# Kernel optimization log

Measured on AMD Instinct MI355X. Metric: run time of the kernel, lower is better.

Reference implementation:

```python
import jax, jax.numpy as jnp
import numpy as np
from jax import lax

H = 128

def _lstm_gates(x, h, c, w_ih, w_hh, b_ih, b_hh):
    # PyTorch gate order: i, f, g, o
    g = x @ w_ih.T + h @ w_hh.T + b_ih + b_hh
    i, f, gg, o = jnp.split(g, 4, axis=-1)
    c_new = jax.nn.sigmoid(f) * c + jax.nn.sigmoid(i) * jnp.tanh(gg)
    h_new = jax.nn.sigmoid(o) * jnp.tanh(c_new)
    return h_new, c_new

def _lstm_layer(x_btF, w_ih, w_hh, b_ih, b_hh):
    B = x_btF.shape[0]
    h0 = jnp.zeros((B, H), x_btF.dtype)
    c0 = jnp.zeros((B, H), x_btF.dtype)
    def step(carry, xt):
        h, c = carry
        h, c = _lstm_gates(xt, h, c, w_ih, w_hh, b_ih, b_hh)
        return (h, c), h
    (h_T, c_T), ys = lax.scan(step, (h0, c0), jnp.swapaxes(x_btF, 0, 1))
    return jnp.swapaxes(ys, 0, 1), h_T, c_T

def setup_inputs() -> dict:
    key = jax.random.key(0)
    ks = jax.random.split(key, 20)
    B, T, D, P = 4096, 200, 2, 3
    s = 1.0 / np.sqrt(H)
    u = lambda k, shp: jax.random.uniform(k, shp, jnp.float32, -s, s)
    return {
        'x_hist': jax.random.normal(ks[0], (B, T, D), jnp.float32),
        'params': jax.random.normal(ks[1], (B, P), jnp.float32),
        'pred_len': 200,
        'w_ih0': u(ks[2], (4 * H, D)), 'w_hh0': u(ks[3], (4 * H, H)),
        'b_ih0': u(ks[4], (4 * H,)), 'b_hh0': u(ks[5], (4 * H,)),
        'w_ih1': u(ks[6], (4 * H, H)), 'w_hh1': u(ks[7], (4 * H, H)),
        'b_ih1': u(ks[8], (4 * H,)), 'b_hh1': u(ks[9], (4 * H,)),
        'dec_w_ih': u(ks[10], (4 * H, D + P)), 'dec_w_hh': u(ks[11], (4 * H, H)),
        'dec_b_ih': u(ks[12], (4 * H,)), 'dec_b_hh': u(ks[13], (4 * H,)),
        'proj_w': u(ks[14], (H, P)), 'proj_b': u(ks[15], (H,)),
        'out_w': u(ks[16], (2, H)), 'out_b': u(ks[17], (2,)),
    }

def reference(x_hist, params, pred_len, w_ih0, w_hh0, b_ih0, b_hh0,
              w_ih1, w_hh1, b_ih1, b_hh1, dec_w_ih, dec_w_hh, dec_b_ih,
              dec_b_hh, proj_w, proj_b, out_w, out_b):
    # 2-layer encoder LSTM; only last layer's final (h, c) are used
    y1, _, _ = _lstm_layer(x_hist, w_ih0, w_hh0, b_ih0, b_hh0)
    _, h_n, c_n = _lstm_layer(y1, w_ih1, w_hh1, b_ih1, b_hh1)
    h = h_n + params @ proj_w.T + proj_b
    c = c_n
    cur = x_hist[:, -1, :]
    def step(carry, _):
        h, c, cur = carry
        inp = jnp.concatenate([cur, params], axis=-1)
        h, c = _lstm_gates(inp, h, c, dec_w_ih, dec_w_hh, dec_b_ih, dec_b_hh)
        cur = h @ out_w.T + out_b
        return (h, c, cur), cur
    _, preds = lax.scan(step, (h, c, cur), None, length=pred_len)
    return jnp.swapaxes(preds, 0, 1)  # [B, pred_len, 2]
```

## Files before the change

### kernel.cpp

```cpp
#include <hip/hip_runtime.h>
#include <stdint.h>

typedef __bf16 bf16x8 __attribute__((ext_vector_type(8)));
typedef float  f32x4  __attribute__((ext_vector_type(4)));

#define PRED   200
#define TSTEPS 200
#define NBLK   256
#define ABUFB  8192
#define L1_A_OFF   131072
#define L1_ST_OFF  (131072 + 2*ABUFB)
#define LDS_L1     (131072 + 3*ABUFB)
#define LDS_SMALL  (2*ABUFB)

#define STATE_FLOATS ((size_t)NBLK*4*2048)

__device__ __forceinline__ float sigm(float x){ return 1.0f/(1.0f+__expf(-x)); }
__device__ __forceinline__ float tanhx(float x){
  float t=__expf(-2.0f*fabsf(x)); float y=(1.0f-t)/(1.0f+t); return copysignf(y,x);
}
__device__ __forceinline__ bf16x8 hi8(float4 a, float4 b){
  bf16x8 r; r[0]=(__bf16)a.x; r[1]=(__bf16)a.y; r[2]=(__bf16)a.z; r[3]=(__bf16)a.w;
  r[4]=(__bf16)b.x; r[5]=(__bf16)b.y; r[6]=(__bf16)b.z; r[7]=(__bf16)b.w; return r;
}
__device__ __forceinline__ bf16x8 lo8(float4 a, float4 b, bf16x8 h){
  bf16x8 r;
  r[0]=(__bf16)(a.x-(float)h[0]); r[1]=(__bf16)(a.y-(float)h[1]);
  r[2]=(__bf16)(a.z-(float)h[2]); r[3]=(__bf16)(a.w-(float)h[3]);
  r[4]=(__bf16)(b.x-(float)h[4]); r[5]=(__bf16)(b.y-(float)h[5]);
  r[6]=(__bf16)(b.z-(float)h[6]); r[7]=(__bf16)(b.w-(float)h[7]); return r;
}
__device__ __forceinline__ uint16_t bfbits(__bf16 x){ union{__bf16 b; uint16_t u;} v; v.b=x; return v.u; }
__device__ __forceinline__ __bf16 bits2bf(uint16_t u){ union{uint16_t u; __bf16 b;} v; v.u=u; return v.b; }
#define MFMA(A,B,C) __builtin_amdgcn_mfma_f32_16x16x32_bf16((A),(B),(C),0,0,0)

__device__ __forceinline__ int aoff(int row, int col){
  return row*512 + ((((col>>3) ^ (row&7)) << 4) | ((col&7)<<1));
}
__device__ __forceinline__ int frdoff(int c, int qd, int kt, int plane){
  return c*512 + (((((kt<<2)+qd) ^ (c&7)) | (plane<<4)) << 4);
}

__global__ void __launch_bounds__(512,1)
k_l0(const float* __restrict__ xh, const float* __restrict__ wih0,
     const float* __restrict__ whh0, const float* __restrict__ bih0,
     const float* __restrict__ bhh0, float* __restrict__ wsf,
     int chunkStart, int chunkLen, unsigned long long stageFloats)
{
  extern __shared__ char smem[];
  const int tid=threadIdx.x, wv=tid>>6, l=tid&63, c=l&15, qd=l>>4;
  const int hc=wv*16+c, blk=blockIdx.x, r0=blk*16;
  float* stf = wsf + stageFloats;
  bf16x8 whi[16], wlo[16];
  #pragma unroll
  for (int tt=0;tt<4;++tt)
    #pragma unroll
    for (int kt=0;kt<4;++kt){
      const float* s=whh0+(size_t)(tt*128+hc)*128+kt*32+qd*8;
      float4 a=*(const float4*)s, b=*(const float4*)(s+4);
      whi[tt*4+kt]=hi8(a,b); wlo[tt*4+kt]=lo8(a,b,whi[tt*4+kt]);
    }
  float b0[4], w0x[4], w0y[4];
  #pragma unroll
  for (int tt=0;tt<4;++tt){
    int g=tt*128+hc;
    b0[tt]=bih0[g]+bhh0[g]; w0x[tt]=wih0[2*g]; w0y[tt]=wih0[2*g+1];
  }
  float c0[4];
  {
    char* B1=smem+ABUFB;
    const float* hst=stf+(size_t)(blk*4+0)*2048;
    const float* cst=stf+(size_t)(blk*4+1)*2048;
    #pragma unroll
    for (int i=0;i<4;++i){
      int e=tid*4+i, row=e>>7, col=e&127;
      float v=0.f; if(chunkStart) v=hst[e];
      __bf16 h=(__bf16)v;
      *(__bf16*)(B1+aoff(row,col))=h;
      *(__bf16*)(B1+aoff(row,col+128))=(__bf16)(v-(float)h);
    }
    #pragma unroll
    for (int j=0;j<4;++j){ float v=0.f; if(chunkStart) v=cst[(qd*4+j)*128+hc]; c0[j]=v; }
  }
  __syncthreads();
  for (int t=0;t<chunkLen;++t){
    const int p=t&1, tg=chunkStart+t;
    float2 xv[4];
    #pragma unroll
    for (int j=0;j<4;++j) xv[j]=*(const float2*)(xh+(size_t)(r0+qd*4+j)*400+tg*2);
    f32x4 acc[4];
    #pragma unroll
    for (int tt=0;tt<4;++tt) acc[tt]=(f32x4){b0[tt],b0[tt],b0[tt],b0[tt]};
    const char* Ar=smem+(size_t)(1-p)*ABUFB;
    #pragma unroll
    for (int kt=0;kt<4;++kt){
      bf16x8 ah=*(const bf16x8*)(Ar+frdoff(c,qd,kt,0));
      bf16x8 al=*(const bf16x8*)(Ar+frdoff(c,qd,kt,1));
      #pragma unroll
      for (int tt=0;tt<4;++tt){
        acc[tt]=MFMA(ah,whi[tt*4+kt],acc[tt]);
        acc[tt]=MFMA(al,whi[tt*4+kt],acc[tt]);
        acc[tt]=MFMA(ah,wlo[tt*4+kt],acc[tt]);
      }
    }
    char* Aw=smem+(size_t)p*ABUFB;
    uint32_t* h0o=(uint32_t*)(wsf+((size_t)t*NBLK+blk)*2048);
    #pragma unroll
    for (int j=0;j<4;++j){
      float gi=acc[0][j]+xv[j].x*w0x[0]+xv[j].y*w0y[0];
      float gf=acc[1][j]+xv[j].x*w0x[1]+xv[j].y*w0y[1];
      float gg=acc[2][j]+xv[j].x*w0x[2]+xv[j].y*w0y[2];
      float go=acc[3][j]+xv[j].x*w0x[3]+xv[j].y*w0y[3];
      float cn=sigm(gf)*c0[j]+sigm(gi)*tanhx(gg); c0[j]=cn;
      float hn=sigm(go)*tanhx(cn);
      int row=qd*4+j;
      __bf16 hh=(__bf16)hn;
      __bf16 hl=(__bf16)(hn-(float)hh);
      *(__bf16*)(Aw+aoff(row,hc))=hh;
      *(__bf16*)(Aw+aoff(row,hc+128))=hl;
      h0o[row*128+hc]=(uint32_t)bfbits(hh) | ((uint32_t)bfbits(hl)<<16);
      if (t==chunkLen-1){
        stf[(size_t)(blk*4+0)*2048+row*128+hc]=hn;
        stf[(size_t)(blk*4+1)*2048+row*128+hc]=cn;
      }
    }
    __syncthreads();
  }
}

__global__ void __launch_bounds__(512,1)
k_l1(const float* __restrict__ wih1, const float* __restrict__ whh1,
     const float* __restrict__ bih1, const float* __restrict__ bhh1,
     float* __restrict__ wsf, int chunkStart, int chunkLen,
     unsigned long long stageFloats)
{
  extern __shared__ char smem[];
  const int tid=threadIdx.x, wv=tid>>6, l=tid&63, c=l&15, qd=l>>4;
  const int hc=wv*16+c, blk=blockIdx.x;
  float* stf = wsf + stageFloats;
  #pragma unroll
  for (int i=0;i<16;++i){
    int f=i*8+wv, ntg=f>>2, kt=f&3;
    int g=(ntg&3)*128+(ntg>>2)*16+c, k=kt*32+qd*8;
    const float* s=wih1+g*128+k;
    *(bf16x8*)(smem+f*1024+l*16)=hi8(*(const float4*)s,*(const float4*)(s+4));
  }
  bf16x8 wil[16], whh[16], whl[16];
  #pragma unroll
  for (int tt=0;tt<4;++tt)
    #pragma unroll
    for (int kt=0;kt<4;++kt){
      const float* s=wih1+(size_t)(tt*128+hc)*128+kt*32+qd*8;
      float4 a=*(const float4*)s, b=*(const float4*)(s+4);
      wil[tt*4+kt]=lo8(a,b,hi8(a,b));
      const float* s2=whh1+(size_t)(tt*128+hc)*128+kt*32+qd*8;
      float4 a2=*(const float4*)s2, b2=*(const float4*)(s2+4);
      bf16x8 h2=hi8(a2,b2);
      whh[tt*4+kt]=h2; whl[tt*4+kt]=lo8(a2,b2,h2);
    }
  float b1v[4];
  #pragma unroll
  for (int tt=0;tt<4;++tt){ int g=tt*128+hc; b1v[tt]=bih1[g]+bhh1[g]; }
  float c1[4];
  {
    char* B1=smem+L1_A_OFF+ABUFB;
    const float* hst=stf+(size_t)(blk*4+2)*2048;
    const float* cst=stf+(size_t)(blk*4+3)*2048;
    #pragma unroll
    for (int i=0;i<4;++i){
      int e=tid*4+i, row=e>>7, col=e&127;
      float v=0.f; if(chunkStart) v=hst[e];
      __bf16 h=(__bf16)v;
      *(__bf16*)(B1+aoff(row,col))=h;
      *(__bf16*)(B1+aoff(row,col+128))=(__bf16)(v-(float)h);
    }
    #pragma unroll
    for (int j=0;j<4;++j){ float v=0.f; if(chunkStart) v=cst[(qd*4+j)*128+hc]; c1[j]=v; }
  }
  uint4 r4=*(const uint4*)((const uint32_t*)(wsf+((size_t)0*NBLK+blk)*2048)+tid*4);
  __syncthreads();
  for (int t=0;t<chunkLen;++t){
    const int p=t&1;
    {
      char* ST=smem+L1_ST_OFF;
      int e=tid*4, row=e>>7, col=e&127;
      uint32_t uu[4]={r4.x,r4.y,r4.z,r4.w};
      #pragma unroll
      for (int i=0;i<4;++i){
        *(__bf16*)(ST+aoff(row,col+i))=bits2bf((uint16_t)(uu[i]&0xFFFFu));
        *(__bf16*)(ST+aoff(row,col+i+128))=bits2bf((uint16_t)(uu[i]>>16));
      }
    }
    if (t+1<chunkLen) r4=*(const uint4*)((const uint32_t*)(wsf+((size_t)(t+1)*NBLK+blk)*2048)+tid*4);
    __syncthreads();
    f32x4 acc[4];
    #pragma unroll
    for (int tt=0;tt<4;++tt) acc[tt]=(f32x4){b1v[tt],b1v[tt],b1v[tt],b1v[tt]};
    const char* Ar=smem+L1_A_OFF+(size_t)(1-p)*ABUFB;
    const char* Sr=smem+L1_ST_OFF;
    #pragma unroll
    for (int kt=0;kt<4;++kt){
      bf16x8 a0h=*(const bf16x8*)(Sr+frdoff(c,qd,kt,0));
      bf16x8 a0l=*(const bf16x8*)(Sr+frdoff(c,qd,kt,1));
      bf16x8 a1h=*(const bf16x8*)(Ar+frdoff(c,qd,kt,0));
      bf16x8 a1l=*(const bf16x8*)(Ar+frdoff(c,qd,kt,1));
      #pragma unroll
      for (int tt=0;tt<4;++tt){
        bf16x8 bh=*(const bf16x8*)(smem+(size_t)((wv*4+tt)*4+kt)*1024+l*16);
        acc[tt]=MFMA(a0h,bh,acc[tt]);
        acc[tt]=MFMA(a0l,bh,acc[tt]);
        acc[tt]=MFMA(a0h,wil[tt*4+kt],acc[tt]);
        acc[tt]=MFMA(a1h,whh[tt*4+kt],acc[tt]);
        acc[tt]=MFMA(a1l,whh[tt*4+kt],acc[tt]);
        acc[tt]=MFMA(a1h,whl[tt*4+kt],acc[tt]);
      }
    }
    char* Aw=smem+L1_A_OFF+(size_t)p*ABUFB;
    #pragma unroll
    for (int j=0;j<4;++j){
      float cn=sigm(acc[1][j])*c1[j]+sigm(acc[0][j])*tanhx(acc[2][j]); c1[j]=cn;
      float hn=sigm(acc[3][j])*tanhx(cn);
      int row=qd*4+j;
      __bf16 hh=(__bf16)hn;
      *(__bf16*)(Aw+aoff(row,hc))=hh;
      *(__bf16*)(Aw+aoff(row,hc+128))=(__bf16)(hn-(float)hh);
      if (t==chunkLen-1){
        stf[(size_t)(blk*4+2)*2048+row*128+hc]=hn;
        stf[(size_t)(blk*4+3)*2048+row*128+hc]=cn;
      }
    }
    __syncthreads();
  }
}

__global__ void __launch_bounds__(512,1)
k_dec(const float* __restrict__ xh, const float* __restrict__ pprm,
      const float* __restrict__ dwihp, const float* __restrict__ dwhh,
      const float* __restrict__ dbih, const float* __restrict__ dbhh,
      const float* __restrict__ pw, const float* __restrict__ pb,
      const float* __restrict__ ow, const float* __restrict__ ob,
      const float* __restrict__ wsf, float* __restrict__ out,
      unsigned long long stageFloats)
{
  extern __shared__ char smem[];
  const int tid=threadIdx.x, wv=tid>>6, l=tid&63, c=l&15, qd=l>>4;
  const int hc=wv*16+c, blk=blockIdx.x, r0=blk*16;
  const float* stf = wsf + stageFloats;
  bf16x8 whi[16], wlo[16];
  #pragma unroll
  for (int tt=0;tt<4;++tt)
    #pragma unroll
    for (int kt=0;kt<4;++kt){
      const float* s=dwhh+(size_t)(tt*128+hc)*128+kt*32+qd*8;
      float4 a=*(const float4*)s, b=*(const float4*)(s+4);
      whi[tt*4+kt]=hi8(a,b); wlo[tt*4+kt]=lo8(a,b,whi[tt*4+kt]);
    }
  bf16x8 owh[4], owl[4];
  #pragma unroll
  for (int kt=0;kt<4;++kt){
    int cc=(c<2)?c:0;
    const float* s=ow+cc*128+kt*32+qd*8;
    float4 a=*(const float4*)s, b=*(const float4*)(s+4);
    if (c>=2){ a=(float4){0,0,0,0}; b=(float4){0,0,0,0}; }
    owh[kt]=hi8(a,b); owl[kt]=lo8(a,b,owh[kt]);
  }
  float ob0=ob[0], ob1=ob[1];
  float prm[4][3];
  #pragma unroll
  for (int j=0;j<4;++j){
    size_t r=(size_t)(r0+qd*4+j);
    prm[j][0]=pprm[r*3+0]; prm[j][1]=pprm[r*3+1]; prm[j][2]=pprm[r*3+2];
  }
  float pt[4][4], dw0[4], dw1[4];
  #pragma unroll
  for (int tt=0;tt<4;++tt){
    int g=tt*128+hc;
    float db=dbih[g]+dbhh[g];
    dw0[tt]=dwihp[g*5+0]; dw1[tt]=dwihp[g*5+1];
    #pragma unroll
    for (int j=0;j<4;++j)
      pt[tt][j]=db+prm[j][0]*dwihp[g*5+2]+prm[j][1]*dwihp[g*5+3]+prm[j][2]*dwihp[g*5+4];
  }
  const float* h1s=stf+(size_t)(blk*4+2)*2048;
  const float* c1s=stf+(size_t)(blk*4+3)*2048;
  float c1[4], cx0[4], cx1[4];
  {
    float prj0=pw[hc*3+0], prj1=pw[hc*3+1], prj2=pw[hc*3+2], prjb=pb[hc];
    char* B0=smem;
    #pragma unroll
    for (int j=0;j<4;++j){
      int row=qd*4+j;
      float hd=h1s[row*128+hc]+prm[j][0]*prj0+prm[j][1]*prj1+prm[j][2]*prj2+prjb;
      __bf16 h=(__bf16)hd;
      *(__bf16*)(B0+aoff(row,hc))=h;
      *(__bf16*)(B0+aoff(row,hc+128))=(__bf16)(hd-(float)h);
      c1[j]=c1s[row*128+hc];
      float2 xx=*(const float2*)(xh+(size_t)(r0+row)*400+398);
      cx0[j]=xx.x; cx1[j]=xx.y;
    }
  }
  __syncthreads();
  for (int s=0;s<PRED;++s){
    const int q=s&1;
    const char* Ar=smem+(size_t)q*ABUFB;
    f32x4 acc[4], accPV={0.f,0.f,0.f,0.f};
    #pragma unroll
    for (int tt=0;tt<4;++tt) acc[tt]=(f32x4){pt[tt][0],pt[tt][1],pt[tt][2],pt[tt][3]};
    #pragma unroll
    for (int kt=0;kt<4;++kt){
      bf16x8 ah=*(const bf16x8*)(Ar+frdoff(c,qd,kt,0));
      bf16x8 al=*(const bf16x8*)(Ar+frdoff(c,qd,kt,1));
      #pragma unroll
      for (int tt=0;tt<4;++tt){
        acc[tt]=MFMA(ah,whi[tt*4+kt],acc[tt]);
        acc[tt]=MFMA(al,whi[tt*4+kt],acc[tt]);
        acc[tt]=MFMA(ah,wlo[tt*4+kt],acc[tt]);
      }
      accPV=MFMA(ah,owh[kt],accPV);
      accPV=MFMA(al,owh[kt],accPV);
      accPV=MFMA(ah,owl[kt],accPV);
    }
    float cur0[4], cur1[4];
    #pragma unroll
    for (int j=0;j<4;++j){
      float pv0=__shfl(accPV[j], (l&48),   64);
      float pv1=__shfl(accPV[j], (l&48)|1, 64);
      cur0[j]= s ? (pv0+ob0) : cx0[j];
      cur1[j]= s ? (pv1+ob1) : cx1[j];
    }
    if (s && wv==0 && c<2){
      float obv=c?ob1:ob0;
      #pragma unroll
      for (int j=0;j<4;++j)
        out[(size_t)(r0+qd*4+j)*400+(s-1)*2+c]=accPV[j]+obv;
    }
    char* Aw=smem+(size_t)(1-q)*ABUFB;
    #pragma unroll
    for (int j=0;j<4;++j){
      float gi=acc[0][j]+cur0[j]*dw0[0]+cur1[j]*dw1[0];
      float gf=acc[1][j]+cur0[j]*dw0[1]+cur1[j]*dw1[1];
      float gg=acc[2][j]+cur0[j]*dw0[2]+cur1[j]*dw1[2];
      float go=acc[3][j]+cur0[j]*dw0[3]+cur1[j]*dw1[3];
      float cn=sigm(gf)*c1[j]+sigm(gi)*tanhx(gg); c1[j]=cn;
      float hn=sigm(go)*tanhx(cn);
      int row=qd*4+j;
      __bf16 hh=(__bf16)hn;
      *(__bf16*)(Aw+aoff(row,hc))=hh;
      *(__bf16*)(Aw+aoff(row,hc+128))=(__bf16)(hn-(float)hh);
    }
    __syncthreads();
  }
  {
    const char* Ar=smem+(size_t)(PRED&1)*ABUFB;
    f32x4 accPV={0.f,0.f,0.f,0.f};
    #pragma unroll
    for (int kt=0;kt<4;++kt){
      bf16x8 ah=*(const bf16x8*)(Ar+frdoff(c,qd,kt,0));
      bf16x8 al=*(const bf16x8*)(Ar+frdoff(c,qd,kt,1));
      accPV=MFMA(ah,owh[kt],accPV);
      accPV=MFMA(al,owh[kt],accPV);
      accPV=MFMA(ah,owl[kt],accPV);
    }
    if (wv==0 && c<2){
      float obv=c?ob1:ob0;
      #pragma unroll
      for (int j=0;j<4;++j)
        out[(size_t)(r0+qd*4+j)*400+(PRED-1)*2+c]=accPV[j]+obv;
    }
  }
}

extern "C" void kernel_launch(void* const* d_in, const int* in_sizes, int n_in,
                              void* d_out, int out_size, void* d_ws, size_t ws_size,
                              hipStream_t stream)
{
  (void)out_size;
  const int base = (n_in >= 19 && in_sizes[2] == 1) ? 3 : 2;
  const float* xh   = (const float*)d_in[0];
  const float* prm  = (const float*)d_in[1];
  const float* wih0 = (const float*)d_in[base+0];
  const float* whh0 = (const float*)d_in[base+1];
  const float* bih0 = (const float*)d_in[base+2];
  const float* bhh0 = (const float*)d_in[base+3];
  const float* wih1 = (const float*)d_in[base+4];
  const float* whh1 = (const float*)d_in[base+5];
  const float* bih1 = (const float*)d_in[base+6];
  const float* bhh1 = (const float*)d_in[base+7];
  const float* dwih = (const float*)d_in[base+8];
  const float* dwhh = (const float*)d_in[base+9];
  const float* dbih = (const float*)d_in[base+10];
  const float* dbhh = (const float*)d_in[base+11];
  const float* pw   = (const float*)d_in[base+12];
  const float* pb   = (const float*)d_in[base+13];
  const float* ow   = (const float*)d_in[base+14];
  const float* ob   = (const float*)d_in[base+15];
  float* wsf = (float*)d_ws;

  size_t wsFloats = ws_size / 4;
  size_t avail = (wsFloats > STATE_FLOATS) ? (wsFloats - STATE_FLOATS) : 0;
  int chunkLen = (int)(avail / ((size_t)NBLK * 2048));
  if (chunkLen > 50) chunkLen = 50;
  if (chunkLen < 1)  chunkLen = 1;
  unsigned long long stageFloats = (unsigned long long)chunkLen * NBLK * 2048;

  hipFuncSetAttribute((const void*)k_l1, hipFuncAttributeMaxDynamicSharedMemorySize, LDS_L1);

  for (int k0 = 0; k0 < TSTEPS; k0 += chunkLen){
    int len = chunkLen; if (k0 + len > TSTEPS) len = TSTEPS - k0;
    k_l0<<<NBLK,512,LDS_SMALL,stream>>>(xh, wih0, whh0, bih0, bhh0, wsf, k0, len, stageFloats);
    k_l1<<<NBLK,512,LDS_L1,stream>>>(wih1, whh1, bih1, bhh1, wsf, k0, len, stageFloats);
  }
  k_dec<<<NBLK,512,LDS_SMALL,stream>>>(xh, prm, dwih, dwhh, dbih, dbhh,
                                       pw, pb, ow, ob, wsf, (float*)d_out, stageFloats);
}
```

Baseline: 2.032 ms.

## Fold decoder output projection into recurrent weights and split MFMA accumulator chains

The decoder now folds the output projection (out_w, out_b) into the recurrent weight matrix and bias, so each step no longer waits on a per-step projection MFMA and shuffle. Projections of the stored bf16 hidden states are computed later in batched sweeps, and a one-time correction term handles the first step's real input. Layer 1 reads layer-0 outputs straight from global memory into registers instead of staging them through LDS with an extra barrier. Both encoder layers and the decoder split their accumulators into two independent chains to shorten MFMA dependency latency. Chunk length is raised to cover all timesteps, which cuts kernel launches when workspace allows. The folded weights and the bf16-only stored hidden state for projection change numerics somewhat.

```diff
diff --git a/kernel.cpp b/kernel.cpp
--- a/kernel.cpp
+++ b/kernel.cpp
@@ -9,8 +9,7 @@
 #define NBLK   256
 #define ABUFB  8192
 #define L1_A_OFF   131072
-#define L1_ST_OFF  (131072 + 2*ABUFB)
-#define LDS_L1     (131072 + 3*ABUFB)
+#define LDS_L1     (131072 + 2*ABUFB)
 #define LDS_SMALL  (2*ABUFB)
 
 #define STATE_FLOATS ((size_t)NBLK*4*2048)
@@ -88,9 +87,9 @@
     float2 xv[4];
     #pragma unroll
     for (int j=0;j<4;++j) xv[j]=*(const float2*)(xh+(size_t)(r0+qd*4+j)*400+tg*2);
-    f32x4 acc[4];
-    #pragma unroll
-    for (int tt=0;tt<4;++tt) acc[tt]=(f32x4){b0[tt],b0[tt],b0[tt],b0[tt]};
+    f32x4 accA[4], accB[4];
+    #pragma unroll
+    for (int tt=0;tt<4;++tt){ accA[tt]=(f32x4){b0[tt],b0[tt],b0[tt],b0[tt]}; accB[tt]=(f32x4){0.f,0.f,0.f,0.f}; }
     const char* Ar=smem+(size_t)(1-p)*ABUFB;
     #pragma unroll
     for (int kt=0;kt<4;++kt){
@@ -98,19 +97,20 @@
       bf16x8 al=*(const bf16x8*)(Ar+frdoff(c,qd,kt,1));
       #pragma unroll
       for (int tt=0;tt<4;++tt){
-        acc[tt]=MFMA(ah,whi[tt*4+kt],acc[tt]);
-        acc[tt]=MFMA(al,whi[tt*4+kt],acc[tt]);
-        acc[tt]=MFMA(ah,wlo[tt*4+kt],acc[tt]);
+        f32x4* tgt=(kt<2)?&accA[tt]:&accB[tt];
+        *tgt=MFMA(ah,whi[tt*4+kt],*tgt);
+        *tgt=MFMA(al,whi[tt*4+kt],*tgt);
+        *tgt=MFMA(ah,wlo[tt*4+kt],*tgt);
       }
     }
     char* Aw=smem+(size_t)p*ABUFB;
     uint32_t* h0o=(uint32_t*)(wsf+((size_t)t*NBLK+blk)*2048);
     #pragma unroll
     for (int j=0;j<4;++j){
-      float gi=acc[0][j]+xv[j].x*w0x[0]+xv[j].y*w0y[0];
-      float gf=acc[1][j]+xv[j].x*w0x[1]+xv[j].y*w0y[1];
-      float gg=acc[2][j]+xv[j].x*w0x[2]+xv[j].y*w0y[2];
-      float go=acc[3][j]+xv[j].x*w0x[3]+xv[j].y*w0y[3];
+      float gi=accA[0][j]+accB[0][j]+xv[j].x*w0x[0]+xv[j].y*w0y[0];
+      float gf=accA[1][j]+accB[1][j]+xv[j].x*w0x[1]+xv[j].y*w0y[1];
+      float gg=accA[2][j]+accB[2][j]+xv[j].x*w0x[2]+xv[j].y*w0y[2];
+      float go=accA[3][j]+accB[3][j]+xv[j].x*w0x[3]+xv[j].y*w0y[3];
       float cn=sigm(gf)*c0[j]+sigm(gi)*tanhx(gg); c0[j]=cn;
       float hn=sigm(go)*tanhx(cn);
       int row=qd*4+j;
@@ -177,49 +177,58 @@
     #pragma unroll
     for (int j=0;j<4;++j){ float v=0.f; if(chunkStart) v=cst[(qd*4+j)*128+hc]; c1[j]=v; }
   }
-  uint4 r4=*(const uint4*)((const uint32_t*)(wsf+((size_t)0*NBLK+blk)*2048)+tid*4);
   __syncthreads();
   for (int t=0;t<chunkLen;++t){
     const int p=t&1;
-    {
-      char* ST=smem+L1_ST_OFF;
-      int e=tid*4, row=e>>7, col=e&127;
-      uint32_t uu[4]={r4.x,r4.y,r4.z,r4.w};
-      #pragma unroll
-      for (int i=0;i<4;++i){
-        *(__bf16*)(ST+aoff(row,col+i))=bits2bf((uint16_t)(uu[i]&0xFFFFu));
-        *(__bf16*)(ST+aoff(row,col+i+128))=bits2bf((uint16_t)(uu[i]>>16));
-      }
-    }
-    if (t+1<chunkLen) r4=*(const uint4*)((const uint32_t*)(wsf+((size_t)(t+1)*NBLK+blk)*2048)+tid*4);
-    __syncthreads();
-    f32x4 acc[4];
-    #pragma unroll
-    for (int tt=0;tt<4;++tt) acc[tt]=(f32x4){b1v[tt],b1v[tt],b1v[tt],b1v[tt]};
+    const uint32_t* h0p=(const uint32_t*)(wsf)+((size_t)t*NBLK+blk)*2048 + c*128 + qd*8;
+    uint4 L[8];
+    #pragma unroll
+    for (int kt=0;kt<4;++kt){
+      L[kt*2]  =*(const uint4*)(h0p+kt*32);
+      L[kt*2+1]=*(const uint4*)(h0p+kt*32+4);
+    }
+    f32x4 acc1[4], acc0[4];
+    #pragma unroll
+    for (int tt=0;tt<4;++tt){ acc1[tt]=(f32x4){b1v[tt],b1v[tt],b1v[tt],b1v[tt]}; acc0[tt]=(f32x4){0.f,0.f,0.f,0.f}; }
     const char* Ar=smem+L1_A_OFF+(size_t)(1-p)*ABUFB;
-    const char* Sr=smem+L1_ST_OFF;
-    #pragma unroll
-    for (int kt=0;kt<4;++kt){
-      bf16x8 a0h=*(const bf16x8*)(Sr+frdoff(c,qd,kt,0));
-      bf16x8 a0l=*(const bf16x8*)(Sr+frdoff(c,qd,kt,1));
+    #pragma unroll
+    for (int kt=0;kt<4;++kt){
       bf16x8 a1h=*(const bf16x8*)(Ar+frdoff(c,qd,kt,0));
       bf16x8 a1l=*(const bf16x8*)(Ar+frdoff(c,qd,kt,1));
       #pragma unroll
       for (int tt=0;tt<4;++tt){
+        acc1[tt]=MFMA(a1h,whh[tt*4+kt],acc1[tt]);
+        acc1[tt]=MFMA(a1l,whh[tt*4+kt],acc1[tt]);
+        acc1[tt]=MFMA(a1h,whl[tt*4+kt],acc1[tt]);
+      }
+    }
+    #pragma unroll
+    for (int kt=0;kt<4;++kt){
+      uint32_t u[8]={L[kt*2].x,L[kt*2].y,L[kt*2].z,L[kt*2].w,
+                     L[kt*2+1].x,L[kt*2+1].y,L[kt*2+1].z,L[kt*2+1].w};
+      bf16x8 a0h, a0l;
+      #pragma unroll
+      for (int i=0;i<8;++i){
+        a0h[i]=bits2bf((uint16_t)(u[i]&0xFFFFu));
+        a0l[i]=bits2bf((uint16_t)(u[i]>>16));
+      }
+      #pragma unroll
+      for (int tt=0;tt<4;++tt){
         bf16x8 bh=*(const bf16x8*)(smem+(size_t)((wv*4+tt)*4+kt)*1024+l*16);
-        acc[tt]=MFMA(a0h,bh,acc[tt]);
-        acc[tt]=MFMA(a0l,bh,acc[tt]);
-        acc[tt]=MFMA(a0h,wil[tt*4+kt],acc[tt]);
-        acc[tt]=MFMA(a1h,whh[tt*4+kt],acc[tt]);
-        acc[tt]=MFMA(a1l,whh[tt*4+kt],acc[tt]);
-        acc[tt]=MFMA(a1h,whl[tt*4+kt],acc[tt]);
+        acc0[tt]=MFMA(a0h,bh,acc0[tt]);
+        acc0[tt]=MFMA(a0l,bh,acc0[tt]);
+        acc0[tt]=MFMA(a0h,wil[tt*4+kt],acc0[tt]);
       }
     }
     char* Aw=smem+L1_A_OFF+(size_t)p*ABUFB;
     #pragma unroll
     for (int j=0;j<4;++j){
-      float cn=sigm(acc[1][j])*c1[j]+sigm(acc[0][j])*tanhx(acc[2][j]); c1[j]=cn;
-      float hn=sigm(acc[3][j])*tanhx(cn);
+      float gi=acc0[0][j]+acc1[0][j];
+      float gf=acc0[1][j]+acc1[1][j];
+      float gg=acc0[2][j]+acc1[2][j];
+      float go=acc0[3][j]+acc1[3][j];
+      float cn=sigm(gf)*c1[j]+sigm(gi)*tanhx(gg); c1[j]=cn;
+      float hn=sigm(go)*tanhx(cn);
       int row=qd*4+j;
       __bf16 hh=(__bf16)hn;
       *(__bf16*)(Aw+aoff(row,hc))=hh;
@@ -239,20 +248,44 @@
       const float* __restrict__ dbih, const float* __restrict__ dbhh,
       const float* __restrict__ pw, const float* __restrict__ pb,
       const float* __restrict__ ow, const float* __restrict__ ob,
-      const float* __restrict__ wsf, float* __restrict__ out,
-      unsigned long long stageFloats)
+      float* __restrict__ wsf, float* __restrict__ out,
+      unsigned long long stageFloats, int hcap)
 {
   extern __shared__ char smem[];
   const int tid=threadIdx.x, wv=tid>>6, l=tid&63, c=l&15, qd=l>>4;
   const int hc=wv*16+c, blk=blockIdx.x, r0=blk*16;
   const float* stf = wsf + stageFloats;
+  float ob0=ob[0], ob1=ob[1];
+  float prm[4][3];
+  #pragma unroll
+  for (int j=0;j<4;++j){
+    size_t r=(size_t)(r0+qd*4+j);
+    prm[j][0]=pprm[r*3+0]; prm[j][1]=pprm[r*3+1]; prm[j][2]=pprm[r*3+2];
+  }
+  float ptF[4][4], dw0[4], dw1[4];
+  #pragma unroll
+  for (int tt=0;tt<4;++tt){
+    int g=tt*128+hc;
+    float db=dbih[g]+dbhh[g];
+    dw0[tt]=dwihp[g*5+0]; dw1[tt]=dwihp[g*5+1];
+    #pragma unroll
+    for (int j=0;j<4;++j)
+      ptF[tt][j]=db+prm[j][0]*dwihp[g*5+2]+prm[j][1]*dwihp[g*5+3]+prm[j][2]*dwihp[g*5+4]
+                 +dw0[tt]*ob0+dw1[tt]*ob1;
+  }
   bf16x8 whi[16], wlo[16];
   #pragma unroll
   for (int tt=0;tt<4;++tt)
     #pragma unroll
     for (int kt=0;kt<4;++kt){
-      const float* s=dwhh+(size_t)(tt*128+hc)*128+kt*32+qd*8;
-      float4 a=*(const float4*)s, b=*(const float4*)(s+4);
+      int g=tt*128+hc, k=kt*32+qd*8;
+      float4 a=*(const float4*)(dwhh+(size_t)g*128+k), b=*(const float4*)(dwhh+(size_t)g*128+k+4);
+      float4 o0a=*(const float4*)(ow+k),     o0b=*(const float4*)(ow+k+4);
+      float4 o1a=*(const float4*)(ow+128+k), o1b=*(const float4*)(ow+128+k+4);
+      a.x+=dw0[tt]*o0a.x+dw1[tt]*o1a.x; a.y+=dw0[tt]*o0a.y+dw1[tt]*o1a.y;
+      a.z+=dw0[tt]*o0a.z+dw1[tt]*o1a.z; a.w+=dw0[tt]*o0a.w+dw1[tt]*o1a.w;
+      b.x+=dw0[tt]*o0b.x+dw1[tt]*o1b.x; b.y+=dw0[tt]*o0b.y+dw1[tt]*o1b.y;
+      b.z+=dw0[tt]*o0b.z+dw1[tt]*o1b.z; b.w+=dw0[tt]*o0b.w+dw1[tt]*o1b.w;
       whi[tt*4+kt]=hi8(a,b); wlo[tt*4+kt]=lo8(a,b,whi[tt*4+kt]);
     }
   bf16x8 owh[4], owl[4];
@@ -263,23 +296,6 @@
     float4 a=*(const float4*)s, b=*(const float4*)(s+4);
     if (c>=2){ a=(float4){0,0,0,0}; b=(float4){0,0,0,0}; }
     owh[kt]=hi8(a,b); owl[kt]=lo8(a,b,owh[kt]);
-  }
-  float ob0=ob[0], ob1=ob[1];
-  float prm[4][3];
-  #pragma unroll
-  for (int j=0;j<4;++j){
-    size_t r=(size_t)(r0+qd*4+j);
-    prm[j][0]=pprm[r*3+0]; prm[j][1]=pprm[r*3+1]; prm[j][2]=pprm[r*3+2];
-  }
-  float pt[4][4], dw0[4], dw1[4];
-  #pragma unroll
-  for (int tt=0;tt<4;++tt){
-    int g=tt*128+hc;
-    float db=dbih[g]+dbhh[g];
-    dw0[tt]=dwihp[g*5+0]; dw1[tt]=dwihp[g*5+1];
-    #pragma unroll
-    for (int j=0;j<4;++j)
-      pt[tt][j]=db+prm[j][0]*dwihp[g*5+2]+prm[j][1]*dwihp[g*5+3]+prm[j][2]*dwihp[g*5+4];
   }
   const float* h1s=stf+(size_t)(blk*4+2)*2048;
   const float* c1s=stf+(size_t)(blk*4+3)*2048;
@@ -300,72 +316,85 @@
     }
   }
   __syncthreads();
+  float corr0[4], corr1[4];
+  {
+    const char* Ar=smem;
+    f32x4 pv={0.f,0.f,0.f,0.f};
+    #pragma unroll
+    for (int kt=0;kt<4;++kt){
+      bf16x8 ah=*(const bf16x8*)(Ar+frdoff(c,qd,kt,0));
+      bf16x8 al=*(const bf16x8*)(Ar+frdoff(c,qd,kt,1));
+      pv=MFMA(ah,owh[kt],pv); pv=MFMA(al,owh[kt],pv); pv=MFMA(ah,owl[kt],pv);
+    }
+    #pragma unroll
+    for (int j=0;j<4;++j){
+      float p0=__shfl(pv[j], (l&48),   64);
+      float p1=__shfl(pv[j], (l&48)|1, 64);
+      corr0[j]=cx0[j]-(p0+ob0);
+      corr1[j]=cx1[j]-(p1+ob1);
+    }
+  }
+  uint16_t* hstp=(uint16_t*)wsf;
+  int sweepBase=0;
   for (int s=0;s<PRED;++s){
     const int q=s&1;
     const char* Ar=smem+(size_t)q*ABUFB;
-    f32x4 acc[4], accPV={0.f,0.f,0.f,0.f};
-    #pragma unroll
-    for (int tt=0;tt<4;++tt) acc[tt]=(f32x4){pt[tt][0],pt[tt][1],pt[tt][2],pt[tt][3]};
+    f32x4 aA[4], aB[4];
+    #pragma unroll
+    for (int tt=0;tt<4;++tt){ aA[tt]=(f32x4){ptF[tt][0],ptF[tt][1],ptF[tt][2],ptF[tt][3]}; aB[tt]=(f32x4){0.f,0.f,0.f,0.f}; }
     #pragma unroll
     for (int kt=0;kt<4;++kt){
       bf16x8 ah=*(const bf16x8*)(Ar+frdoff(c,qd,kt,0));
       bf16x8 al=*(const bf16x8*)(Ar+frdoff(c,qd,kt,1));
       #pragma unroll
       for (int tt=0;tt<4;++tt){
-        acc[tt]=MFMA(ah,whi[tt*4+kt],acc[tt]);
-        acc[tt]=MFMA(al,whi[tt*4+kt],acc[tt]);
-        acc[tt]=MFMA(ah,wlo[tt*4+kt],acc[tt]);
-      }
-      accPV=MFMA(ah,owh[kt],accPV);
-      accPV=MFMA(al,owh[kt],accPV);
-      accPV=MFMA(ah,owl[kt],accPV);
-    }
-    float cur0[4], cur1[4];
+        f32x4* tgt=(kt<2)?&aA[tt]:&aB[tt];
+        *tgt=MFMA(ah,whi[tt*4+kt],*tgt);
+        *tgt=MFMA(al,whi[tt*4+kt],*tgt);
+        *tgt=MFMA(ah,wlo[tt*4+kt],*tgt);
+      }
+    }
+    char* Aw=smem+(size_t)(1-q)*ABUFB;
+    uint16_t* hs=hstp+(size_t)(s-sweepBase)*((size_t)NBLK*2048)+(size_t)blk*2048;
     #pragma unroll
     for (int j=0;j<4;++j){
-      float pv0=__shfl(accPV[j], (l&48),   64);
-      float pv1=__shfl(accPV[j], (l&48)|1, 64);
-      cur0[j]= s ? (pv0+ob0) : cx0[j];
-      cur1[j]= s ? (pv1+ob1) : cx1[j];
-    }
-    if (s && wv==0 && c<2){
-      float obv=c?ob1:ob0;
-      #pragma unroll
-      for (int j=0;j<4;++j)
-        out[(size_t)(r0+qd*4+j)*400+(s-1)*2+c]=accPV[j]+obv;
-    }
-    char* Aw=smem+(size_t)(1-q)*ABUFB;
-    #pragma unroll
-    for (int j=0;j<4;++j){
-      float gi=acc[0][j]+cur0[j]*dw0[0]+cur1[j]*dw1[0];
-      float gf=acc[1][j]+cur0[j]*dw0[1]+cur1[j]*dw1[1];
-      float gg=acc[2][j]+cur0[j]*dw0[2]+cur1[j]*dw1[2];
-      float go=acc[3][j]+cur0[j]*dw0[3]+cur1[j]*dw1[3];
+      float gi=aA[0][j]+aB[0][j];
+      float gf=aA[1][j]+aB[1][j];
+      float gg=aA[2][j]+aB[2][j];
+      float go=aA[3][j]+aB[3][j];
+      if (s==0){
+        gi+=corr0[j]*dw0[0]+corr1[j]*dw1[0];
+        gf+=corr0[j]*dw0[1]+corr1[j]*dw1[1];
+        gg+=corr0[j]*dw0[2]+corr1[j]*dw1[2];
+        go+=corr0[j]*dw0[3]+corr1[j]*dw1[3];
+      }
       float cn=sigm(gf)*c1[j]+sigm(gi)*tanhx(gg); c1[j]=cn;
       float hn=sigm(go)*tanhx(cn);
       int row=qd*4+j;
       __bf16 hh=(__bf16)hn;
       *(__bf16*)(Aw+aoff(row,hc))=hh;
       *(__bf16*)(Aw+aoff(row,hc+128))=(__bf16)(hn-(float)hh);
+      hs[row*128+hc]=bfbits(hh);
     }
     __syncthreads();
-  }
-  {
-    const char* Ar=smem+(size_t)(PRED&1)*ABUFB;
-    f32x4 accPV={0.f,0.f,0.f,0.f};
-    #pragma unroll
-    for (int kt=0;kt<4;++kt){
-      bf16x8 ah=*(const bf16x8*)(Ar+frdoff(c,qd,kt,0));
-      bf16x8 al=*(const bf16x8*)(Ar+frdoff(c,qd,kt,1));
-      accPV=MFMA(ah,owh[kt],accPV);
-      accPV=MFMA(al,owh[kt],accPV);
-      accPV=MFMA(ah,owl[kt],accPV);
-    }
-    if (wv==0 && c<2){
-      float obv=c?ob1:ob0;
-      #pragma unroll
-      for (int j=0;j<4;++j)
-        out[(size_t)(r0+qd*4+j)*400+(PRED-1)*2+c]=accPV[j]+obv;
+    if (s+1-sweepBase==hcap || s==PRED-1){
+      for (int sc=sweepBase+wv; sc<=s; sc+=8){
+        const uint16_t* hp=hstp+(size_t)(sc-sweepBase)*((size_t)NBLK*2048)+(size_t)blk*2048;
+        f32x4 pv={0.f,0.f,0.f,0.f};
+        #pragma unroll
+        for (int kt=0;kt<4;++kt){
+          bf16x8 ah=*(const bf16x8*)(hp+c*128+kt*32+qd*8);
+          pv=MFMA(ah,owh[kt],pv); pv=MFMA(ah,owl[kt],pv);
+        }
+        if (c<2){
+          float obv=c?ob1:ob0;
+          #pragma unroll
+          for (int j=0;j<4;++j)
+            out[(size_t)(r0+qd*4+j)*400+sc*2+c]=pv[j]+obv;
+        }
+      }
+      __syncthreads();
+      sweepBase=s+1;
     }
   }
 }
@@ -399,9 +428,12 @@
   size_t wsFloats = ws_size / 4;
   size_t avail = (wsFloats > STATE_FLOATS) ? (wsFloats - STATE_FLOATS) : 0;
   int chunkLen = (int)(avail / ((size_t)NBLK * 2048));
-  if (chunkLen > 50) chunkLen = 50;
+  if (chunkLen > TSTEPS) chunkLen = TSTEPS;
   if (chunkLen < 1)  chunkLen = 1;
   unsigned long long stageFloats = (unsigned long long)chunkLen * NBLK * 2048;
+  int hcap = (int)(stageFloats / ((size_t)NBLK * 1024));
+  if (hcap > PRED) hcap = PRED;
+  if (hcap < 1) hcap = 1;
 
   hipFuncSetAttribute((const void*)k_l1, hipFuncAttributeMaxDynamicSharedMemorySize, LDS_L1);
 
@@ -411,5 +443,5 @@
     k_l1<<<NBLK,512,LDS_L1,stream>>>(wih1, whh1, bih1, bhh1, wsf, k0, len, stageFloats);
   }
   k_dec<<<NBLK,512,LDS_SMALL,stream>>>(xh, prm, dwih, dwhh, dbih, dbhh,
-                                       pw, pb, ow, ob, wsf, (float*)d_out, stageFloats);
-}
+                                       pw, pb, ow, ob, wsf, (float*)d_out, stageFloats, hcap);
+}
```

Measured after the change: 2.440 ms. 1.2x slower.
